# Kernel tuning notes

Hardware: AMD Instinct MI355X
Metric: run time of the kernel (lower is better)

## Reference

```python
import jax, jax.numpy as jnp
import numpy as np

S, N, C_M, C_Z, C, H = 256, 384, 64, 128, 32, 8


def _layer_norm(x, w, b, eps=1e-5):
    mu = x.mean(axis=-1, keepdims=True)
    var = x.var(axis=-1, keepdims=True)
    return (x - mu) / jnp.sqrt(var + eps) * w + b


def setup_inputs() -> dict:
    key = jax.random.key(0)
    ks = jax.random.split(key, 8)
    m = jax.random.normal(ks[0], (S, N, C_M), dtype=jnp.float32)
    z = jax.random.normal(ks[1], (N, N, C_Z), dtype=jnp.float32)
    single_mask = jax.random.bernoulli(ks[2], 0.9, (N,))
    scale = 0.02
    return {
        "m": m,
        "z": z,
        "single_mask": single_mask,
        "ln_m_w": jnp.ones((C_M,), jnp.float32),
        "ln_m_b": jnp.zeros((C_M,), jnp.float32),
        "ln_z_w": jnp.ones((C_Z,), jnp.float32),
        "ln_z_b": jnp.zeros((C_Z,), jnp.float32),
        "w_v": jax.random.normal(ks[3], (C_M, H * C), jnp.float32) * scale,
        "w_b": jax.random.normal(ks[4], (C_Z, H), jnp.float32) * scale,
        "w_g": jax.random.normal(ks[5], (C_M, H * C), jnp.float32) * scale,
        "w_out": jax.random.normal(ks[6], (H * C, C_M), jnp.float32) * scale,
    }


def reference(m, z, single_mask, ln_m_w, ln_m_b, ln_z_w, ln_z_b, w_v, w_b, w_g, w_out):
    # m: [s, i, c_m], z: [i, j, c_z], single_mask: [j] bool
    m_ln = _layer_norm(m, ln_m_w, ln_m_b)
    v = (m_ln @ w_v).reshape(S, N, H, C)          # [s, j, h, c]
    b = _layer_norm(z, ln_z_w, ln_z_b) @ w_b      # [i, j, h]
    g = jax.nn.sigmoid(m_ln @ w_g)                # [s, i, h*c]
    # mask broadcast over j axis: [..., None, :, None]
    b = b + jnp.where(single_mask[None, :, None], 0.0, -1e9)
    w = jax.nn.softmax(b, axis=-2)                # softmax over j
    o = jnp.einsum('ijh,sjhc->sihc', w, v)        # [s, i, h, c]
    o = g * o.reshape(S, N, H * C)
    return o @ w_out                               # [s, i, c_m]
```

## Files before the change

### kernel.cpp

```cpp
#include <hip/hip_runtime.h>
#include <math.h>


#define SS 256
#define NN 384
#define CM 64
#define CZ 128
#define HH 8
#define HC 256
#define NV 25165824

typedef __attribute__((ext_vector_type(8))) short short8v;
typedef __attribute__((ext_vector_type(8))) unsigned short ushort8v;
typedef __attribute__((ext_vector_type(4))) unsigned short ushort4v;
typedef __attribute__((ext_vector_type(4))) float f32x4;

static __device__ __forceinline__ float bf2f(unsigned short u) {
    union { unsigned int i; float f; } x; x.i = ((unsigned int)u) << 16; return x.f;
}
static __device__ __forceinline__ unsigned short f2bf(float f) {
    union { float f; unsigned int i; } x; x.f = f;
    unsigned int r = x.i + 0x7FFFu + ((x.i >> 16) & 1u);
    return (unsigned short)(r >> 16);
}
static __device__ __forceinline__ void gload_lds16(const void* g, void* l) {
    __builtin_amdgcn_global_load_lds((const __attribute__((address_space(1))) void*)g,
                                     (__attribute__((address_space(3))) void*)l, 16, 0, 0);
}

__global__ __launch_bounds__(384) void k0_mask(const unsigned int* __restrict__ mu,
                                               float* __restrict__ mterm)
{
    __shared__ int byteLayout;
    if (threadIdx.x == 0) byteLayout = 0;
    __syncthreads();
    if (threadIdx.x < 96) {
        unsigned int u = mu[threadIdx.x];
        if (u != 0u && u != 1u && u != 0x3F800000u) atomicOr(&byteLayout, 1);
    }
    __syncthreads();
    const int j = threadIdx.x;
    int val;
    if (byteLayout) val = ((const unsigned char*)mu)[j];
    else            val = (mu[j] != 0u);
    mterm[j] = val ? 0.0f : -1e9f;
}

__global__ __launch_bounds__(256) void k1a_stageB(
    const float* __restrict__ w_v, const float* __restrict__ w_g,
    unsigned short* __restrict__ BTg)
{
    const int col = blockIdx.x * 4 + (threadIdx.x >> 6);
    const int k   = threadIdx.x & 63;
    float w = (col < 256) ? w_v[k * 256 + col] : w_g[k * 256 + (col - 256)];
    BTg[col * 64 + (k ^ ((col & 7) << 3))] = f2bf(w);
}

__global__ __launch_bounds__(128) void k2a_stageW(
    const float* __restrict__ lnw, const float* __restrict__ lnb, const float* __restrict__ w_b,
    unsigned short* __restrict__ w2bf, float* __restrict__ consts)
{
    __shared__ float pA[128][8], pB[128][8];
    const int c = threadIdx.x;
    float lw = lnw[c], lb = lnb[c];
    float4 wb0 = *(const float4*)&w_b[c * 8];
    float4 wb1 = *(const float4*)&w_b[c * 8 + 4];
    float wv[8] = {wb0.x, wb0.y, wb0.z, wb0.w, wb1.x, wb1.y, wb1.z, wb1.w};
    #pragma unroll
    for (int h = 0; h < 8; h++) {
        w2bf[h * CZ + c]       = f2bf(lw * wv[h]);
        w2bf[(8 + h) * CZ + c] = 0;
        pA[c][h] = lw * wv[h];
        pB[c][h] = lb * wv[h];
    }
    __syncthreads();
    if (c < 8) {
        float A = 0.f, B = 0.f;
        for (int q = 0; q < 128; q++) { A += pA[q][c]; B += pB[q][c]; }
        consts[c] = A; consts[16 + c] = B;
        consts[8 + c] = 0.f; consts[24 + c] = 0.f;
    }
}

__global__ __launch_bounds__(256) void k1n_ln(
    const float* __restrict__ m, const float* __restrict__ lnw, const float* __restrict__ lnb,
    unsigned short* __restrict__ mln)
{
    const int tid = threadIdx.x, wid = tid >> 6, lane = tid & 63;
    const int rowBase = blockIdx.x * 64 + wid * 16;
    const float lw = lnw[lane], lb = lnb[lane];
    #pragma unroll 4
    for (int rr = 0; rr < 16; rr++) {
        int row = rowBase + rr;
        float x = m[(size_t)row * CM + lane];
        float s1 = x, s2 = x * x;
        #pragma unroll
        for (int off = 32; off; off >>= 1) {
            s1 += __shfl_xor(s1, off);
            s2 += __shfl_xor(s2, off);
        }
        float mu  = s1 * (1.0f / CM);
        float var = s2 * (1.0f / CM) - mu * mu;
        float y = (x - mu) * rsqrtf(var + 1e-5f) * lw + lb;
        mln[(size_t)row * CM + (lane ^ ((row & 7) << 3))] = f2bf(y);
    }
}

__global__ __launch_bounds__(256) void k1b_vg(
    const unsigned short* __restrict__ BTg, const unsigned short* __restrict__ mln,
    unsigned short* __restrict__ vT, unsigned short* __restrict__ gout)
{
    __shared__ unsigned short Wl[32768];
    __shared__ unsigned short Al[4096];
    const int tid = threadIdx.x, wid = tid >> 6, lane = tid & 63;
    const int rl = lane & 15, kc = lane >> 4;
    const int rowBase = blockIdx.x * 64;
    const int s = rowBase / NN, j0 = rowBase - s * NN;

    #pragma unroll
    for (int it = 0; it < 8; it++) {
        int eoff = wid * 4096 + it * 512;
        gload_lds16(BTg + eoff + lane * 8, (void*)((char*)Wl + eoff * 2));
    }
    #pragma unroll
    for (int it = 0; it < 8; it++) {
        int eoff = 16384 + wid * 4096 + it * 512;
        gload_lds16(BTg + eoff + lane * 8, (void*)((char*)Wl + eoff * 2));
    }
    #pragma unroll
    for (int it = 0; it < 8; it++) {
        int eoff = it * 512;
        gload_lds16(mln + (size_t)rowBase * CM + eoff + lane * 8, (void*)((char*)Al + eoff * 2));
    }
    asm volatile("s_waitcnt vmcnt(0)" ::: "memory");
    __builtin_amdgcn_sched_barrier(0);

    short8v al[2][4];
    #pragma unroll
    for (int ks = 0; ks < 2; ks++)
        #pragma unroll
        for (int q = 0; q < 4; q++) {
            int row = q * 16 + rl;
            al[ks][q] = *(const short8v*)&Al[(row * 64 + ks * 32 + kc * 8) ^ ((row & 7) << 3)];
        }

    unsigned short* VS = Wl + wid * 4096;

    {
        f32x4 acc[4][4] = {};
        #pragma unroll
        for (int ks = 0; ks < 2; ks++) {
            short8v wf[4];
            #pragma unroll
            for (int q = 0; q < 4; q++) {
                int col = wid * 64 + q * 16 + rl;
                wf[q] = *(const short8v*)&Wl[(col * 64 + ks * 32 + kc * 8) ^ ((col & 7) << 3)];
            }
            #pragma unroll
            for (int mi = 0; mi < 4; mi++)
                #pragma unroll
                for (int nf = 0; nf < 4; nf++)
                    acc[mi][nf] = __builtin_amdgcn_mfma_f32_16x16x32_bf16(al[ks][mi], wf[nf], acc[mi][nf], 0, 0, 0);
        }
        #pragma unroll
        for (int mi = 0; mi < 4; mi++) {
            const int jb = mi * 16 + kc * 4;
            #pragma unroll
            for (int nf = 0; nf < 4; nf++) {
                int hcl = nf * 16 + rl;
                ushort4v o4;
                #pragma unroll
                for (int r = 0; r < 4; r++) o4[r] = f2bf(acc[mi][nf][r]);
                *(ushort4v*)&VS[(hcl * 64 + jb) ^ ((hcl & 7) << 3)] = o4;
            }
        }
        #pragma unroll
        for (int p = 0; p < 8; p++) {
            int hcl = p * 8 + (lane >> 3);
            int j8  = (lane & 7) * 8;
            ushort8v val = *(const ushort8v*)&VS[(hcl * 64 + j8) ^ ((hcl & 7) << 3)];
            int hc = wid * 64 + hcl;
            size_t vrow = (size_t)((hc >> 5) * 8192 + s * 32 + (hc & 31));
            *(ushort8v*)&vT[vrow * NN + j0 + j8] = val;
        }
    }

    {
        f32x4 acc[4][4] = {};
        #pragma unroll
        for (int ks = 0; ks < 2; ks++) {
            short8v wf[4];
            #pragma unroll
            for (int q = 0; q < 4; q++) {
                int col = 256 + wid * 64 + q * 16 + rl;
                wf[q] = *(const short8v*)&Wl[(col * 64 + ks * 32 + kc * 8) ^ ((col & 7) << 3)];
            }
            #pragma unroll
            for (int mi = 0; mi < 4; mi++)
                #pragma unroll
                for (int nf = 0; nf < 4; nf++)
                    acc[mi][nf] = __builtin_amdgcn_mfma_f32_16x16x32_bf16(wf[mi], al[ks][nf], acc[mi][nf], 0, 0, 0);
        }
        #pragma unroll
        for (int mi = 0; mi < 4; mi++) {
            const int hcb = mi * 16 + kc * 4;
            #pragma unroll
            for (int nf = 0; nf < 4; nf++) {
                int rowl = nf * 16 + rl;
                ushort4v o4;
                #pragma unroll
                for (int r = 0; r < 4; r++)
                    o4[r] = f2bf(1.0f / (1.0f + __expf(-acc[mi][nf][r])));
                *(ushort4v*)&VS[(rowl * 64 + hcb) ^ ((rowl & 7) << 3)] = o4;
            }
        }
        #pragma unroll
        for (int p = 0; p < 8; p++) {
            int rowl = p * 8 + (lane >> 3);
            int hc8  = (lane & 7) * 8;
            ushort8v val = *(const ushort8v*)&VS[(rowl * 64 + hc8) ^ ((rowl & 7) << 3)];
            *(ushort8v*)&gout[(size_t)(rowBase + rowl) * HC + wid * 64 + hc8] = val;
        }
    }
}

__global__ __launch_bounds__(256) void k2_mfma(
    const float* __restrict__ z, const unsigned short* __restrict__ w2bf,
    const float* __restrict__ consts, const float* __restrict__ mterm,
    unsigned short* __restrict__ wbl)
{
    __shared__ float st[4][16][2];
    const int tid = threadIdx.x, wid = tid >> 6, lane = tid & 63;
    const int rl = lane & 15, kc = lane >> 4;
    const int rowBase = blockIdx.x * 64 + wid * 16;
    const int i = rowBase / NN, j0 = rowBase - i * NN;
    const float* zr = z + (size_t)(rowBase + rl) * CZ + kc * 8;

    float s1 = 0.f, s2 = 0.f;
    short8v af[4];
    #pragma unroll
    for (int ks = 0; ks < 4; ks++) {
        float4 z0 = *(const float4*)(zr + ks * 32);
        float4 z1 = *(const float4*)(zr + ks * 32 + 4);
        float zz[8] = {z0.x, z0.y, z0.z, z0.w, z1.x, z1.y, z1.z, z1.w};
        short8v a;
        #pragma unroll
        for (int q = 0; q < 8; q++) {
            s1 += zz[q];
            s2 += zz[q] * zz[q];
            a[q] = (short)f2bf(zz[q]);
        }
        af[ks] = a;
    }
    s1 += __shfl_xor(s1, 16); s2 += __shfl_xor(s2, 16);
    s1 += __shfl_xor(s1, 32); s2 += __shfl_xor(s2, 32);
    if (kc == 0) { st[wid][rl][0] = s1; st[wid][rl][1] = s2; }

    f32x4 acc = {};
    #pragma unroll
    for (int ks = 0; ks < 4; ks++) {
        short8v b = *(const short8v*)&w2bf[rl * CZ + ks * 32 + kc * 8];
        acc = __builtin_amdgcn_mfma_f32_16x16x32_bf16(af[ks], b, acc, 0, 0, 0);
    }
    __syncthreads();

    const float Ah = consts[rl], Bh = consts[16 + rl];
    unsigned short pv[4];
    #pragma unroll
    for (int reg = 0; reg < 4; reg++) {
        int r = 4 * kc + reg;
        float S1 = st[wid][r][0], S2 = st[wid][r][1];
        float mu   = S1 * (1.0f / CZ);
        float var  = S2 * (1.0f / CZ) - mu * mu;
        float rstd = rsqrtf(var + 1e-5f);
        float b = rstd * acc[reg] - rstd * mu * Ah + Bh + mterm[j0 + r];
        pv[reg] = f2bf(b);
    }
    if (rl < 8) {
        ushort4v o4 = {pv[0], pv[1], pv[2], pv[3]};
        *(ushort4v*)&wbl[((size_t)rl * NN + i) * NN + j0 + 4 * kc] = o4;
    }
}

__global__ __launch_bounds__(256) void k3_softmax(unsigned short* __restrict__ wbl)
{
    const int tid = threadIdx.x, wave = tid >> 6, lane = tid & 63;
    const int row = blockIdx.x * 4 + wave;
    unsigned short* p = wbl + (size_t)row * NN;
    float x[6];
    float mx = -1e30f;
    #pragma unroll
    for (int e = 0; e < 6; e++) { x[e] = bf2f(p[lane + e * 64]); mx = fmaxf(mx, x[e]); }
    #pragma unroll
    for (int off = 32; off; off >>= 1) mx = fmaxf(mx, __shfl_xor(mx, off));
    float sum = 0.f;
    #pragma unroll
    for (int e = 0; e < 6; e++) { x[e] = expf(x[e] - mx); sum += x[e]; }
    #pragma unroll
    for (int off = 32; off; off >>= 1) sum += __shfl_xor(sum, off);
    float inv = 1.0f / sum;
    #pragma unroll
    for (int e = 0; e < 6; e++) p[lane + e * 64] = f2bf(x[e] * inv);
}

__global__ __launch_bounds__(256) void k4_mfma(
    const unsigned short* __restrict__ wbf, const unsigned short* __restrict__ vT,
    unsigned short* __restrict__ ob)
{
    __shared__ unsigned short Al[128 * 32];
    __shared__ unsigned short Bl[128 * 32];
    const int tid  = threadIdx.x;
    const int wid  = tid >> 6, lane = tid & 63;
    const int wm   = wid >> 1, wn = wid & 1;
    const int h    = blockIdx.z;
    const int i0   = blockIdx.y * 128;
    const int n0   = blockIdx.x * 128;
    const unsigned short* Ag = wbf + (size_t)h * NN * NN;
    const unsigned short* Bg = vT  + (size_t)h * 8192 * NN;

    f32x4 acc[4][4] = {};

    const int lrow = lane >> 2, lchunk = lane & 3;
    for (int k0 = 0; k0 < NN; k0 += 32) {
        #pragma unroll
        for (int q = 0; q < 2; q++) {
            int issue = wid * 2 + q;
            int r = issue * 16 + lrow;
            gload_lds16(Ag + (size_t)(i0 + r) * NN + k0 + lchunk * 8,
                        (void*)((char*)Al + issue * 1024));
            gload_lds16(Bg + (size_t)(n0 + r) * NN + k0 + lchunk * 8,
                        (void*)((char*)Bl + issue * 1024));
        }
        __syncthreads();

        short8v a[4], b[4];
        #pragma unroll
        for (int mi = 0; mi < 4; mi++)
            a[mi] = *(const short8v*)&Al[(wm * 64 + mi * 16 + (lane & 15)) * 32 + (lane >> 4) * 8];
        #pragma unroll
        for (int ni = 0; ni < 4; ni++)
            b[ni] = *(const short8v*)&Bl[(wn * 64 + ni * 16 + (lane & 15)) * 32 + (lane >> 4) * 8];
        #pragma unroll
        for (int mi = 0; mi < 4; mi++)
            #pragma unroll
            for (int ni = 0; ni < 4; ni++)
                acc[mi][ni] = __builtin_amdgcn_mfma_f32_16x16x32_bf16(a[mi], b[ni], acc[mi][ni], 0, 0, 0);
        __syncthreads();
    }

    #pragma unroll
    for (int mi = 0; mi < 4; mi++) {
        const int ibase = i0 + wm * 64 + mi * 16 + ((lane >> 4) << 2);
        #pragma unroll
        for (int ni = 0; ni < 4; ni++) {
            const int n = n0 + wn * 64 + ni * 16 + (lane & 15);
            const int s = n >> 5, c = n & 31;
            #pragma unroll
            for (int r = 0; r < 4; r++)
                ob[((size_t)s * NN + (ibase + r)) * HC + (h << 5) + c] = f2bf(acc[mi][ni][r]);
        }
    }
}

__global__ __launch_bounds__(256) void k5_mfma(
    const unsigned short* __restrict__ ob, const unsigned short* __restrict__ g,
    const float* __restrict__ w_out, float* __restrict__ out)
{
    __shared__ unsigned short WT[64 * 256];
    const int tid = threadIdx.x, wid = tid >> 6, lane = tid & 63;
    #pragma unroll
    for (int e = 0; e < 16; e++) {
        int fidx = (tid + e * 256) * 4;
        float4 w4 = *(const float4*)&w_out[fidx];
        int k = fidx >> 6, c0 = fidx & 63;
        float wv[4] = {w4.x, w4.y, w4.z, w4.w};
        #pragma unroll
        for (int q = 0; q < 4; q++) {
            int c = c0 + q;
            WT[(((c << 8) + k)) ^ ((c & 7) << 3)] = f2bf(wv[q]);
        }
    }
    __syncthreads();

    const size_t rowbase = (size_t)blockIdx.x * 64 + wid * 16;
    const int arow = lane & 15, achunk = lane >> 4;
    const unsigned short* op = ob + (rowbase + arow) * HC + achunk * 8;
    const unsigned short* gp = g  + (rowbase + arow) * HC + achunk * 8;

    f32x4 acc[4] = {};
    #pragma unroll
    for (int ks = 0; ks < 8; ks++) {
        ushort8v o8 = *(const ushort8v*)(op + ks * 32);
        ushort8v g8 = *(const ushort8v*)(gp + ks * 32);
        short8v a;
        #pragma unroll
        for (int q = 0; q < 8; q++)
            a[q] = (short)f2bf(bf2f(o8[q]) * bf2f(g8[q]));
        #pragma unroll
        for (int nf = 0; nf < 4; nf++) {
            const int c = nf * 16 + arow;
            short8v b = *(const short8v*)&WT[(((c << 8) + ks * 32 + achunk * 8)) ^ ((c & 7) << 3)];
            acc[nf] = __builtin_amdgcn_mfma_f32_16x16x32_bf16(a, b, acc[nf], 0, 0, 0);
        }
    }
    #pragma unroll
    for (int nf = 0; nf < 4; nf++)
        #pragma unroll
        for (int r = 0; r < 4; r++)
            out[(rowbase + achunk * 4 + r) * CM + nf * 16 + arow] = acc[nf][r];
}

extern "C" void kernel_launch(void* const* d_in, const int* in_sizes, int n_in,
                              void* d_out, int out_size, void* d_ws, size_t ws_size,
                              hipStream_t stream)
{
    const float* m      = (const float*)d_in[0];
    const float* z      = (const float*)d_in[1];
    const unsigned int* mask_raw = (const unsigned int*)d_in[2];
    const float* ln_m_w = (const float*)d_in[3];
    const float* ln_m_b = (const float*)d_in[4];
    const float* ln_z_w = (const float*)d_in[5];
    const float* ln_z_b = (const float*)d_in[6];
    const float* w_v    = (const float*)d_in[7];
    const float* w_b    = (const float*)d_in[8];
    const float* w_g    = (const float*)d_in[9];
    const float* w_out  = (const float*)d_in[10];
    float* out = (float*)d_out;

    float* mterm = (float*)d_ws;
    unsigned short* wbl = (unsigned short*)(mterm + 384);
    unsigned short* vT  = wbl + 1179648;
    unsigned short* g   = vT + NV;
    unsigned short* ob  = g + NV;
    unsigned short* BTg = ob + NV;
    unsigned short* w2bf = BTg + 32768;
    float* consts = (float*)(w2bf + 2048);
    unsigned short* mln = ob;

    k0_mask<<<1, 384, 0, stream>>>(mask_raw, mterm);
    k1a_stageB<<<128, 256, 0, stream>>>(w_v, w_g, BTg);
    k2a_stageW<<<1, 128, 0, stream>>>(ln_z_w, ln_z_b, w_b, w2bf, consts);
    k1n_ln<<<1536, 256, 0, stream>>>(m, ln_m_w, ln_m_b, mln);
    k1b_vg<<<1536, 256, 0, stream>>>(BTg, mln, vT, g);
    k2_mfma<<<2304, 256, 0, stream>>>(z, w2bf, consts, mterm, wbl);
    k3_softmax<<<768, 256, 0, stream>>>(wbl);
    k4_mfma<<<dim3(64, 3, 8), 256, 0, stream>>>(wbl, vT, ob);
    k5_mfma<<<1536, 256, 0, stream>>>(ob, g, w_out, out);
}
```

Measured before the change: 134.7 us.

## Fuse m LayerNorm into v/g projection kernel and split v/g across grid y

Removes the separate LayerNorm kernel and its bf16 mln round-trip through global memory. Each projection block now loads its 64 rows of m directly, computes the LayerNorm in registers and writes the result into LDS. The grid gains a second dimension so one block handles either the v or the g projection. This halves the per-block weight LDS footprint but duplicates the LayerNorm work and m reads across the two families.

```diff
diff --git a/kernel.cpp b/kernel.cpp
--- a/kernel.cpp
+++ b/kernel.cpp
@@ -82,56 +82,52 @@
     }
 }
 
-__global__ __launch_bounds__(256) void k1n_ln(
-    const float* __restrict__ m, const float* __restrict__ lnw, const float* __restrict__ lnb,
-    unsigned short* __restrict__ mln)
-{
-    const int tid = threadIdx.x, wid = tid >> 6, lane = tid & 63;
-    const int rowBase = blockIdx.x * 64 + wid * 16;
-    const float lw = lnw[lane], lb = lnb[lane];
-    #pragma unroll 4
-    for (int rr = 0; rr < 16; rr++) {
-        int row = rowBase + rr;
-        float x = m[(size_t)row * CM + lane];
-        float s1 = x, s2 = x * x;
-        #pragma unroll
-        for (int off = 32; off; off >>= 1) {
-            s1 += __shfl_xor(s1, off);
-            s2 += __shfl_xor(s2, off);
-        }
-        float mu  = s1 * (1.0f / CM);
-        float var = s2 * (1.0f / CM) - mu * mu;
-        float y = (x - mu) * rsqrtf(var + 1e-5f) * lw + lb;
-        mln[(size_t)row * CM + (lane ^ ((row & 7) << 3))] = f2bf(y);
-    }
-}
-
 __global__ __launch_bounds__(256) void k1b_vg(
-    const unsigned short* __restrict__ BTg, const unsigned short* __restrict__ mln,
+    const unsigned short* __restrict__ BTg, const float* __restrict__ m,
+    const float* __restrict__ lnw, const float* __restrict__ lnb,
     unsigned short* __restrict__ vT, unsigned short* __restrict__ gout)
 {
-    __shared__ unsigned short Wl[32768];
+    __shared__ unsigned short Wl[16384];
     __shared__ unsigned short Al[4096];
     const int tid = threadIdx.x, wid = tid >> 6, lane = tid & 63;
     const int rl = lane & 15, kc = lane >> 4;
     const int rowBase = blockIdx.x * 64;
     const int s = rowBase / NN, j0 = rowBase - s * NN;
+    const int fam = blockIdx.y;
+
+    float mx[16];
+    #pragma unroll
+    for (int rr = 0; rr < 16; rr++)
+        mx[rr] = m[(size_t)(rowBase + wid * 16 + rr) * CM + lane];
+    __builtin_amdgcn_sched_barrier(0);
 
     #pragma unroll
     for (int it = 0; it < 8; it++) {
         int eoff = wid * 4096 + it * 512;
-        gload_lds16(BTg + eoff + lane * 8, (void*)((char*)Wl + eoff * 2));
-    }
-    #pragma unroll
-    for (int it = 0; it < 8; it++) {
-        int eoff = 16384 + wid * 4096 + it * 512;
-        gload_lds16(BTg + eoff + lane * 8, (void*)((char*)Wl + eoff * 2));
-    }
-    #pragma unroll
-    for (int it = 0; it < 8; it++) {
-        int eoff = it * 512;
-        gload_lds16(mln + (size_t)rowBase * CM + eoff + lane * 8, (void*)((char*)Al + eoff * 2));
-    }
+        gload_lds16(BTg + fam * 16384 + eoff + lane * 8, (void*)((char*)Wl + eoff * 2));
+    }
+    __builtin_amdgcn_sched_barrier(0);
+
+    const float lw = lnw[lane], lb = lnb[lane];
+    #pragma unroll
+    for (int rr = 0; rr < 16; rr++) {
+        int row = wid * 16 + rr;
+        float x = mx[rr];
+        float s1 = x, s2 = x * x;
+        #pragma unroll
+        for (int off = 32; off; off >>= 1) {
+            s1 += __shfl_xor(s1, off);
+            s2 += __shfl_xor(s2, off);
+        }
+        float mu  = s1 * (1.0f / CM);
+        float var = s2 * (1.0f / CM) - mu * mu;
+        float y = (x - mu) * rsqrtf(var + 1e-5f) * lw + lb;
+        Al[row * 64 + (lane ^ ((row & 7) << 3))] = f2bf(y);
+    }
+
+    asm volatile("s_waitcnt lgkmcnt(0)" ::: "memory");
+    __builtin_amdgcn_s_barrier();
+    __builtin_amdgcn_sched_barrier(0);
     asm volatile("s_waitcnt vmcnt(0)" ::: "memory");
     __builtin_amdgcn_sched_barrier(0);
 
@@ -146,7 +142,7 @@
 
     unsigned short* VS = Wl + wid * 4096;
 
-    {
+    if (fam == 0) {
         f32x4 acc[4][4] = {};
         #pragma unroll
         for (int ks = 0; ks < 2; ks++) {
@@ -183,16 +179,14 @@
             size_t vrow = (size_t)((hc >> 5) * 8192 + s * 32 + (hc & 31));
             *(ushort8v*)&vT[vrow * NN + j0 + j8] = val;
         }
-    }
-
-    {
+    } else {
         f32x4 acc[4][4] = {};
         #pragma unroll
         for (int ks = 0; ks < 2; ks++) {
             short8v wf[4];
             #pragma unroll
             for (int q = 0; q < 4; q++) {
-                int col = 256 + wid * 64 + q * 16 + rl;
+                int col = wid * 64 + q * 16 + rl;
                 wf[q] = *(const short8v*)&Wl[(col * 64 + ks * 32 + kc * 8) ^ ((col & 7) << 3)];
             }
             #pragma unroll
@@ -435,13 +429,11 @@
     unsigned short* BTg = ob + NV;
     unsigned short* w2bf = BTg + 32768;
     float* consts = (float*)(w2bf + 2048);
-    unsigned short* mln = ob;
 
     k0_mask<<<1, 384, 0, stream>>>(mask_raw, mterm);
     k1a_stageB<<<128, 256, 0, stream>>>(w_v, w_g, BTg);
     k2a_stageW<<<1, 128, 0, stream>>>(ln_z_w, ln_z_b, w_b, w2bf, consts);
-    k1n_ln<<<1536, 256, 0, stream>>>(m, ln_m_w, ln_m_b, mln);
-    k1b_vg<<<1536, 256, 0, stream>>>(BTg, mln, vT, g);
+    k1b_vg<<<dim3(1536, 2), 256, 0, stream>>>(BTg, m, ln_m_w, ln_m_b, vT, g);
     k2_mfma<<<2304, 256, 0, stream>>>(z, w2bf, consts, mterm, wbl);
     k3_softmax<<<768, 256, 0, stream>>>(wbl);
     k4_mfma<<<dim3(64, 3, 8), 256, 0, stream>>>(wbl, vT, ob);
```

After: 138.6 us. 1.03x slower.

## Merge prep kernels into one launch and vectorize k4 output stores

Applied to the files above, without the earlier changes.

Combines the three small setup kernels (mask, bias weight staging, V/G weight transpose) into a single launch whose blocks branch on blockIdx, removing two kernel launches and their gaps. In k4, the MFMA operands are swapped so each lane holds four consecutive channel values for one row, which lets the epilogue write 8-byte ushort4 vectors instead of scattered 2-byte stores. The fused prep kernel uses divergent per-block roles and shared memory declared inside branches, so its LDS footprint is the union for every block.

```diff
diff --git a/kernel.cpp b/kernel.cpp
--- a/kernel.cpp
+++ b/kernel.cpp
@@ -28,57 +28,57 @@
                                      (__attribute__((address_space(3))) void*)l, 16, 0, 0);
 }
 
-__global__ __launch_bounds__(384) void k0_mask(const unsigned int* __restrict__ mu,
-                                               float* __restrict__ mterm)
-{
-    __shared__ int byteLayout;
-    if (threadIdx.x == 0) byteLayout = 0;
-    __syncthreads();
-    if (threadIdx.x < 96) {
-        unsigned int u = mu[threadIdx.x];
-        if (u != 0u && u != 1u && u != 0x3F800000u) atomicOr(&byteLayout, 1);
-    }
-    __syncthreads();
-    const int j = threadIdx.x;
-    int val;
-    if (byteLayout) val = ((const unsigned char*)mu)[j];
-    else            val = (mu[j] != 0u);
-    mterm[j] = val ? 0.0f : -1e9f;
-}
-
-__global__ __launch_bounds__(256) void k1a_stageB(
+__global__ __launch_bounds__(256) void k_prep(
+    const unsigned int* __restrict__ mu, const float* __restrict__ lnzw,
+    const float* __restrict__ lnzb, const float* __restrict__ w_b,
     const float* __restrict__ w_v, const float* __restrict__ w_g,
-    unsigned short* __restrict__ BTg)
-{
-    const int col = blockIdx.x * 4 + (threadIdx.x >> 6);
-    const int k   = threadIdx.x & 63;
-    float w = (col < 256) ? w_v[k * 256 + col] : w_g[k * 256 + (col - 256)];
-    BTg[col * 64 + (k ^ ((col & 7) << 3))] = f2bf(w);
-}
-
-__global__ __launch_bounds__(128) void k2a_stageW(
-    const float* __restrict__ lnw, const float* __restrict__ lnb, const float* __restrict__ w_b,
-    unsigned short* __restrict__ w2bf, float* __restrict__ consts)
-{
-    __shared__ float pA[128][8], pB[128][8];
-    const int c = threadIdx.x;
-    float lw = lnw[c], lb = lnb[c];
-    float4 wb0 = *(const float4*)&w_b[c * 8];
-    float4 wb1 = *(const float4*)&w_b[c * 8 + 4];
-    float wv[8] = {wb0.x, wb0.y, wb0.z, wb0.w, wb1.x, wb1.y, wb1.z, wb1.w};
-    #pragma unroll
-    for (int h = 0; h < 8; h++) {
-        w2bf[h * CZ + c]       = f2bf(lw * wv[h]);
-        w2bf[(8 + h) * CZ + c] = 0;
-        pA[c][h] = lw * wv[h];
-        pB[c][h] = lb * wv[h];
-    }
-    __syncthreads();
-    if (c < 8) {
-        float A = 0.f, B = 0.f;
-        for (int q = 0; q < 128; q++) { A += pA[q][c]; B += pB[q][c]; }
-        consts[c] = A; consts[16 + c] = B;
-        consts[8 + c] = 0.f; consts[24 + c] = 0.f;
+    float* __restrict__ mterm, unsigned short* __restrict__ w2bf,
+    float* __restrict__ consts, unsigned short* __restrict__ BTg)
+{
+    const int b = blockIdx.x, tid = threadIdx.x;
+    if (b == 0) {
+        __shared__ int byteLayout;
+        if (tid == 0) byteLayout = 0;
+        __syncthreads();
+        if (tid < 96) {
+            unsigned int u = mu[tid];
+            if (u != 0u && u != 1u && u != 0x3F800000u) atomicOr(&byteLayout, 1);
+        }
+        __syncthreads();
+        for (int j = tid; j < 384; j += 256) {
+            int val;
+            if (byteLayout) val = ((const unsigned char*)mu)[j];
+            else            val = (mu[j] != 0u);
+            mterm[j] = val ? 0.0f : -1e9f;
+        }
+    } else if (b == 1) {
+        __shared__ float pA[128][8], pB[128][8];
+        const int c = tid & 127;
+        if (tid < 128) {
+            float lw = lnzw[c], lb = lnzb[c];
+            float4 wb0 = *(const float4*)&w_b[c * 8];
+            float4 wb1 = *(const float4*)&w_b[c * 8 + 4];
+            float wv[8] = {wb0.x, wb0.y, wb0.z, wb0.w, wb1.x, wb1.y, wb1.z, wb1.w};
+            #pragma unroll
+            for (int h = 0; h < 8; h++) {
+                w2bf[h * CZ + c]       = f2bf(lw * wv[h]);
+                w2bf[(8 + h) * CZ + c] = 0;
+                pA[c][h] = lw * wv[h];
+                pB[c][h] = lb * wv[h];
+            }
+        }
+        __syncthreads();
+        if (tid < 8) {
+            float A = 0.f, B = 0.f;
+            for (int q = 0; q < 128; q++) { A += pA[q][tid]; B += pB[q][tid]; }
+            consts[tid] = A; consts[16 + tid] = B;
+            consts[8 + tid] = 0.f; consts[24 + tid] = 0.f;
+        }
+    } else {
+        const int col = (b - 2) * 4 + (tid >> 6);
+        const int k   = tid & 63;
+        float w = (col < 256) ? w_v[k * 256 + col] : w_g[k * 256 + (col - 256)];
+        BTg[col * 64 + (k ^ ((col & 7) << 3))] = f2bf(w);
     }
 }
 
@@ -344,20 +344,21 @@
         for (int mi = 0; mi < 4; mi++)
             #pragma unroll
             for (int ni = 0; ni < 4; ni++)
-                acc[mi][ni] = __builtin_amdgcn_mfma_f32_16x16x32_bf16(a[mi], b[ni], acc[mi][ni], 0, 0, 0);
+                acc[mi][ni] = __builtin_amdgcn_mfma_f32_16x16x32_bf16(b[ni], a[mi], acc[mi][ni], 0, 0, 0);
         __syncthreads();
     }
 
     #pragma unroll
     for (int mi = 0; mi < 4; mi++) {
-        const int ibase = i0 + wm * 64 + mi * 16 + ((lane >> 4) << 2);
+        const int i = i0 + wm * 64 + mi * 16 + (lane & 15);
         #pragma unroll
         for (int ni = 0; ni < 4; ni++) {
-            const int n = n0 + wn * 64 + ni * 16 + (lane & 15);
-            const int s = n >> 5, c = n & 31;
-            #pragma unroll
-            for (int r = 0; r < 4; r++)
-                ob[((size_t)s * NN + (ibase + r)) * HC + (h << 5) + c] = f2bf(acc[mi][ni][r]);
+            const int sc0 = n0 + wn * 64 + ni * 16 + ((lane >> 4) << 2);
+            const int s = sc0 >> 5, c0 = sc0 & 31;
+            ushort4v o4;
+            #pragma unroll
+            for (int r = 0; r < 4; r++) o4[r] = f2bf(acc[mi][ni][r]);
+            *(ushort4v*)&ob[((size_t)s * NN + i) * HC + (h << 5) + c0] = o4;
         }
     }
 }
@@ -437,9 +438,8 @@
     float* consts = (float*)(w2bf + 2048);
     unsigned short* mln = ob;
 
-    k0_mask<<<1, 384, 0, stream>>>(mask_raw, mterm);
-    k1a_stageB<<<128, 256, 0, stream>>>(w_v, w_g, BTg);
-    k2a_stageW<<<1, 128, 0, stream>>>(ln_z_w, ln_z_b, w_b, w2bf, consts);
+    k_prep<<<130, 256, 0, stream>>>(mask_raw, ln_z_w, ln_z_b, w_b, w_v, w_g,
+                                    mterm, w2bf, consts, BTg);
     k1n_ln<<<1536, 256, 0, stream>>>(m, ln_m_w, ln_m_b, mln);
     k1b_vg<<<1536, 256, 0, stream>>>(BTg, mln, vT, g);
     k2_mfma<<<2304, 256, 0, stream>>>(z, w2bf, consts, mterm, wbl);
```

New measurement: 134.3 us, median of 2. Within noise of the previous version (-0.2%).
